# Kernel tuning notes

Hardware: AMD Instinct MI355X
Metric: run time of the kernel (lower is better)

Reference implementation:

```python
import jax, jax.numpy as jnp
import numpy as np

# Problem sizes (batched graph of G molecules)
N = 100_000   # total nodes
E = 400_000   # total directed edges
G = 2_500     # number of molecule graphs
K = 3         # len(idx_wo_smiles) -> zero rows inserted
NODE_F = 74   # graph_feats_shape[0]
EDGE_F = 12   # graph_feats_shape[1]
HID = 128     # hidden_feats = dim // 2
DIM = 256     # dim


def setup_inputs() -> dict:
    key = jax.random.key(0)
    ks = jax.random.split(key, 20)
    init = lambda k, shape, fan: (jax.random.normal(k, shape, jnp.float32) / np.sqrt(fan)).astype(jnp.float32)

    node_feats = jax.random.normal(ks[0], (N, NODE_F), jnp.float32)
    edge_feats = jax.random.normal(ks[1], (E, EDGE_F), jnp.float32)  # passed but unused by GCN
    src = jax.random.randint(ks[2], (E,), 0, N)
    dst = jax.random.randint(ks[3], (E,), 0, N)
    # sorted graph ids, every graph non-empty (~40 atoms each)
    graph_ids = (jnp.arange(N) * G) // N
    idx_wo_smiles = jnp.arange(K)

    return {
        'node_feats': node_feats,
        'edge_feats': edge_feats,
        'W1': init(ks[4], (NODE_F, HID), NODE_F), 'b1': jnp.zeros((HID,), jnp.float32),
        'Wr1': init(ks[5], (NODE_F, HID), NODE_F), 'br1': jnp.zeros((HID,), jnp.float32),
        'W2': init(ks[6], (HID, HID), HID), 'b2': jnp.zeros((HID,), jnp.float32),
        'Wr2': init(ks[7], (HID, HID), HID), 'br2': jnp.zeros((HID,), jnp.float32),
        'w_atom': init(ks[8], (HID, 1), HID), 'b_atom': jnp.zeros((1,), jnp.float32),
        'Wp1': init(ks[9], (2 * HID, HID), 2 * HID), 'bp1': jnp.zeros((HID,), jnp.float32),
        'Wp2': init(ks[10], (HID, DIM), HID), 'bp2': jnp.zeros((DIM,), jnp.float32),
        'src': src, 'dst': dst, 'graph_ids': graph_ids, 'idx_wo_smiles': idx_wo_smiles,
    }


def reference(node_feats, edge_feats, W1, b1, Wr1, br1, W2, b2, Wr2, br2,
              w_atom, b_atom, Wp1, bp1, Wp2, bp2, src, dst, graph_ids, idx_wo_smiles):
    n = node_feats.shape[0]
    ones_e = jnp.ones(src.shape[0], jnp.float32)
    out_deg = jax.ops.segment_sum(ones_e, src, num_segments=n)
    in_deg = jax.ops.segment_sum(ones_e, dst, num_segments=n)
    norm_s = jax.lax.rsqrt(jnp.maximum(out_deg, 1.0))  # [N]
    norm_d = jax.lax.rsqrt(jnp.maximum(in_deg, 1.0))   # [N]

    def gcn_layer(h, W, b, Wr, br):
        # GraphConv(norm='both'): D^-1/2 A D^-1/2 h W + b, with relu activation
        m = h[src] * norm_s[src][:, None]                       # [E, F] gather
        agg = jax.ops.segment_sum(m, dst, num_segments=n)       # [N, F] scatter-add
        gc = jax.nn.relu((agg * norm_d[:, None]) @ W + b)
        res = jax.nn.relu(h @ Wr + br)                          # residual connection
        return gc + res

    h = gcn_layer(node_feats, W1, b1, Wr1, br1)   # [N, HID]
    h = gcn_layer(h, W2, b2, Wr2, br2)            # [N, HID]

    # WeightedSumAndMax readout per molecule
    aw = jax.nn.sigmoid(h @ w_atom + b_atom)                          # [N, 1]
    hsum = jax.ops.segment_sum(h * aw, graph_ids, num_segments=G)     # [G, HID]
    hmax = jax.ops.segment_max(h, graph_ids, num_segments=G)          # [G, HID]
    gfeat = jnp.concatenate([hsum, hmax], axis=1)                     # [G, 2*HID]

    latent = jax.nn.relu(gfeat @ Wp1 + bp1) @ Wp2 + bp2               # [G, DIM]

    # Insert zero rows at idx_wo_smiles (sorted ascending -> final positions)
    total = G + idx_wo_smiles.shape[0]
    zero_mask = jnp.zeros((total,), bool).at[idx_wo_smiles].set(True)
    keep = jnp.nonzero(~zero_mask, size=G)[0]
    out = jnp.zeros((total, latent.shape[1]), latent.dtype).at[keep].set(latent)
    return out
```

## Files before the change

kernel.cpp:

```cpp
#include <hip/hip_runtime.h>
#include <hip/hip_bf16.h>

#define NODE_F 74
#define HID 128
#define DIM 256

typedef __hip_bfloat16 bf16;
typedef unsigned int u32;
typedef unsigned short u16;

typedef short s16x8 __attribute__((ext_vector_type(8)));
typedef __bf16 bf16x8 __attribute__((ext_vector_type(8)));
typedef float f32x4 __attribute__((ext_vector_type(4)));

__device__ __forceinline__ float rdl(float v, int l){
  return __int_as_float(__builtin_amdgcn_readlane(__float_as_int(v), l));
}
__device__ __forceinline__ float2 bfpair(u32 u){
  float2 r;
  r.x = __uint_as_float(u << 16);
  r.y = __uint_as_float(u & 0xffff0000u);
  return r;
}
__device__ __forceinline__ u16 bfbits(float a){
  return __bfloat16_as_ushort(__float2bfloat16(a));
}

__global__ void k_deg(const int* __restrict__ src, const int* __restrict__ dst,
                      float* __restrict__ outdeg_f, int* __restrict__ indeg, int E_){
  int e = blockIdx.x*256 + threadIdx.x;
  if (e < E_){
    atomicAdd(&outdeg_f[src[e]], 1.0f);
    atomicAdd(&indeg[dst[e]], 1);
  }
}

__global__ void k_norm(float* __restrict__ norm_s, const int* __restrict__ indeg,
                       float* __restrict__ norm_d, int n){
  int i = blockIdx.x*256 + threadIdx.x;
  if (i < n){
    norm_s[i] = rsqrtf(fmaxf(norm_s[i], 1.0f));
    norm_d[i] = rsqrtf(fmaxf((float)indeg[i], 1.0f));
  }
}

__global__ __launch_bounds__(256) void k_scan_a(const int* __restrict__ indeg,
                                                int* __restrict__ bsum, int n){
  __shared__ int red[256];
  const int base = blockIdx.x*1024 + threadIdx.x*4;
  int s = 0;
  #pragma unroll
  for (int i = 0; i < 4; ++i){
    const int idx = base + i;
    s += (idx < n) ? indeg[idx] : 0;
  }
  red[threadIdx.x] = s;
  __syncthreads();
  #pragma unroll
  for (int off = 128; off; off >>= 1){
    if (threadIdx.x < off) red[threadIdx.x] += red[threadIdx.x + off];
    __syncthreads();
  }
  if (threadIdx.x == 0) bsum[blockIdx.x] = red[0];
}

__global__ __launch_bounds__(1024) void k_scan_b(int* __restrict__ bsum, int nb){
  __shared__ int part[1024];
  __shared__ int carry;
  if (threadIdx.x == 0) carry = 0;
  __syncthreads();
  for (int c0 = 0; c0 < nb; c0 += 1024){
    const int tid = threadIdx.x, idx = c0 + tid;
    part[tid] = (idx < nb) ? bsum[idx] : 0;
    __syncthreads();
    for (int off = 1; off < 1024; off <<= 1){
      const int t = (tid >= off) ? part[tid-off] : 0;
      __syncthreads();
      part[tid] += t;
      __syncthreads();
    }
    if (idx < nb) bsum[idx] = carry + ((tid == 0) ? 0 : part[tid-1]);
    __syncthreads();
    if (tid == 0) carry += part[1023];
    __syncthreads();
  }
}

__global__ __launch_bounds__(256) void k_scan_c(int* __restrict__ indeg,
                                                const int* __restrict__ bsum,
                                                int* __restrict__ row_ptr, int n){
  __shared__ int part[256];
  const int base = blockIdx.x*1024 + threadIdx.x*4;
  int v[4]; int s = 0;
  #pragma unroll
  for (int i = 0; i < 4; ++i){
    const int idx = base + i;
    v[i] = (idx < n) ? indeg[idx] : 0;
    s += v[i];
  }
  part[threadIdx.x] = s;
  __syncthreads();
  for (int off = 1; off < 256; off <<= 1){
    const int t = (threadIdx.x >= off) ? part[threadIdx.x-off] : 0;
    __syncthreads();
    part[threadIdx.x] += t;
    __syncthreads();
  }
  int run = bsum[blockIdx.x] + ((threadIdx.x == 0) ? 0 : part[threadIdx.x-1]);
  #pragma unroll
  for (int i = 0; i < 4; ++i){
    const int idx = base + i;
    if (idx < n){
      row_ptr[idx] = run;
      run += v[i];
      indeg[idx] = 0;
    }
    if (idx == n-1) row_ptr[n] = run;
  }
}

__global__ void k_fill(const int* __restrict__ src, const int* __restrict__ dst,
                       const int* __restrict__ row_ptr, int* __restrict__ cursor,
                       int* __restrict__ col, int E_){
  int e = blockIdx.x*256 + threadIdx.x;
  if (e < E_){
    int d = dst[e];
    int pos = row_ptr[d] + atomicAdd(&cursor[d], 1);
    col[pos] = src[e];
  }
}

__global__ void k_prep(const float* __restrict__ W, u16* __restrict__ dst,
                       int S, int Ktrue){
  int idx = blockIdx.x*256 + threadIdx.x;
  const int tot = 8*S*512;
  if (idx >= tot) return;
  const int e   = idx & 7;
  const int l   = (idx >> 3) & 63;
  const int rem = idx >> 9;
  const int s   = rem % S;
  const int t   = rem / S;
  const int k   = s*32 + (l >> 4)*8 + e;
  const int c   = t*16 + (l & 15);
  const float v = (k < Ktrue) ? W[(size_t)k*HID + c] : 0.f;
  dst[idx] = bfbits(v);
}

__global__ __launch_bounds__(256) void k_fgemm1(
    const float* __restrict__ x0, const int* __restrict__ row_ptr,
    const int* __restrict__ col, const float* __restrict__ norm_s,
    const float* __restrict__ norm_d,
    const u16* __restrict__ Bp, const float* __restrict__ bg_,
    const float* __restrict__ br_, u16* __restrict__ h1, int n){
  const int lane = threadIdx.x & 63;
  const int wid  = threadIdx.x >> 6;
  const int jg = lane & 15, kg = lane >> 4;
  const int r0 = blockIdx.x*64 + wid*16;
  const int row = r0 + jg;
  const bool rok = row < n;
  const int kb = kg*8;

  float agg[3][8];
  #pragma unroll
  for (int s = 0; s < 3; ++s)
    #pragma unroll
    for (int e = 0; e < 8; ++e) agg[s][e] = 0.f;

  auto accum = [&](const float* px, float ns){
    #pragma unroll
    for (int s = 0; s < 2; ++s){
      #pragma unroll
      for (int e = 0; e < 8; e += 2){
        const float2 v = *(const float2*)&px[s*32 + kb + e];
        agg[s][e]   = fmaf(v.x, ns, agg[s][e]);
        agg[s][e+1] = fmaf(v.y, ns, agg[s][e+1]);
      }
    }
    if (kg == 0){
      #pragma unroll
      for (int e = 0; e < 8; e += 2){
        const float2 v = *(const float2*)&px[64 + e];
        agg[2][e]   = fmaf(v.x, ns, agg[2][e]);
        agg[2][e+1] = fmaf(v.y, ns, agg[2][e+1]);
      }
    } else if (kg == 1){
      const float2 v = *(const float2*)&px[72];
      agg[2][0] = fmaf(v.x, ns, agg[2][0]);
      agg[2][1] = fmaf(v.y, ns, agg[2][1]);
    }
  };

  int p0 = 0, p1 = 0;
  if (rok){ p0 = row_ptr[row]; p1 = row_ptr[row+1]; }
  int p = p0;
  #pragma unroll 1
  for (; p + 1 < p1; p += 2){
    const int sa = col[p], sb = col[p+1];
    const float na = norm_s[sa], nb = norm_s[sb];
    const float* xa = x0 + (size_t)sa*NODE_F;
    const float* xb = x0 + (size_t)sb*NODE_F;
    accum(xa, na);
    accum(xb, nb);
  }
  if (p < p1){
    const int sa = col[p];
    accum(x0 + (size_t)sa*NODE_F, norm_s[sa]);
  }

  const float nd = rok ? norm_d[row] : 0.f;
  bf16x8 ag[3], ar[3];
  #pragma unroll
  for (int s = 0; s < 3; ++s)
    #pragma unroll
    for (int e = 0; e < 8; ++e) ag[s][e] = (__bf16)(agg[s][e]*nd);

  {
    const int rA = rok ? row : (n-1);
    const float* px = x0 + (size_t)rA*NODE_F;
    #pragma unroll
    for (int s = 0; s < 2; ++s)
      #pragma unroll
      for (int e = 0; e < 8; e += 2){
        const float2 w = *(const float2*)&px[s*32 + kb + e];
        ar[s][e]   = (__bf16)w.x;
        ar[s][e+1] = (__bf16)w.y;
      }
    #pragma unroll
    for (int e = 0; e < 8; ++e) ar[2][e] = (__bf16)0.f;
    if (kg == 0){
      #pragma unroll
      for (int e = 0; e < 8; e += 2){
        const float2 w = *(const float2*)&px[64 + e];
        ar[2][e]   = (__bf16)w.x;
        ar[2][e+1] = (__bf16)w.y;
      }
    } else if (kg == 1){
      const float2 w = *(const float2*)&px[72];
      ar[2][0] = (__bf16)w.x;
      ar[2][1] = (__bf16)w.y;
    }
  }

  f32x4 accg[8], accr[8];
  #pragma unroll
  for (int t = 0; t < 8; ++t){
    accg[t] = f32x4{0.f,0.f,0.f,0.f};
    accr[t] = f32x4{0.f,0.f,0.f,0.f};
  }
  constexpr int FR1 = 8*3*512;
  #pragma unroll
  for (int s = 0; s < 3; ++s){
    #pragma unroll
    for (int t = 0; t < 8; ++t){
      const bf16x8 bg = __builtin_bit_cast(bf16x8,
          *(const s16x8*)&Bp[((t*3 + s)*64 + lane)*8]);
      const bf16x8 br = __builtin_bit_cast(bf16x8,
          *(const s16x8*)&Bp[FR1 + ((t*3 + s)*64 + lane)*8]);
      accg[t] = __builtin_amdgcn_mfma_f32_16x16x32_bf16(ag[s], bg, accg[t], 0,0,0);
      accr[t] = __builtin_amdgcn_mfma_f32_16x16x32_bf16(ar[s], br, accr[t], 0,0,0);
    }
  }

  const int rowb = r0 + 4*kg;
  #pragma unroll
  for (int t = 0; t < 8; ++t){
    const int colc = t*16 + jg;
    const float bgv = bg_[colc], brv = br_[colc];
    #pragma unroll
    for (int r = 0; r < 4; ++r){
      const int row2 = rowb + r;
      if (row2 < n){
        const float o = fmaxf(accg[t][r] + bgv, 0.f) + fmaxf(accr[t][r] + brv, 0.f);
        h1[(size_t)row2*HID + colc] = bfbits(o);
      }
    }
  }
}

__global__ __launch_bounds__(256) void k_fgemm2(
    const u16* __restrict__ h1, const int* __restrict__ row_ptr,
    const int* __restrict__ col, const float* __restrict__ norm_s,
    const float* __restrict__ norm_d,
    const u16* __restrict__ Bp, const float* __restrict__ bg_,
    const float* __restrict__ br_,
    const float* __restrict__ w_atom, const float* __restrict__ b_atom,
    const int* __restrict__ gid,
    float* __restrict__ hsum, u32* __restrict__ hmax, int n){
  const int lane = threadIdx.x & 63;
  const int wid  = threadIdx.x >> 6;
  const int jg = lane & 15, kg = lane >> 4;
  const int r0 = blockIdx.x*64 + wid*16;
  const int row = r0 + jg;
  const bool rok = row < n;
  const int kb = kg*8;

  float agg[4][8];
  #pragma unroll
  for (int s = 0; s < 4; ++s)
    #pragma unroll
    for (int e = 0; e < 8; ++e) agg[s][e] = 0.f;

  auto accum = [&](uint4 v, int s, float ns){
    const float2 f0 = bfpair(v.x), f1 = bfpair(v.y);
    const float2 f2 = bfpair(v.z), f3 = bfpair(v.w);
    agg[s][0] = fmaf(f0.x, ns, agg[s][0]);
    agg[s][1] = fmaf(f0.y, ns, agg[s][1]);
    agg[s][2] = fmaf(f1.x, ns, agg[s][2]);
    agg[s][3] = fmaf(f1.y, ns, agg[s][3]);
    agg[s][4] = fmaf(f2.x, ns, agg[s][4]);
    agg[s][5] = fmaf(f2.y, ns, agg[s][5]);
    agg[s][6] = fmaf(f3.x, ns, agg[s][6]);
    agg[s][7] = fmaf(f3.y, ns, agg[s][7]);
  };

  int p0 = 0, p1 = 0;
  if (rok){ p0 = row_ptr[row]; p1 = row_ptr[row+1]; }
  int p = p0;
  #pragma unroll 1
  for (; p + 1 < p1; p += 2){
    const int sa = col[p], sb = col[p+1];
    const float na = norm_s[sa], nb = norm_s[sb];
    const u16* pa = h1 + (size_t)sa*HID + kb;
    const u16* pb = h1 + (size_t)sb*HID + kb;
    const uint4 va0 = *(const uint4*)(pa);
    const uint4 va1 = *(const uint4*)(pa + 32);
    const uint4 va2 = *(const uint4*)(pa + 64);
    const uint4 va3 = *(const uint4*)(pa + 96);
    const uint4 vb0 = *(const uint4*)(pb);
    const uint4 vb1 = *(const uint4*)(pb + 32);
    const uint4 vb2 = *(const uint4*)(pb + 64);
    const uint4 vb3 = *(const uint4*)(pb + 96);
    accum(va0, 0, na); accum(va1, 1, na); accum(va2, 2, na); accum(va3, 3, na);
    accum(vb0, 0, nb); accum(vb1, 1, nb); accum(vb2, 2, nb); accum(vb3, 3, nb);
  }
  if (p < p1){
    const int sa = col[p];
    const float na = norm_s[sa];
    const u16* pa = h1 + (size_t)sa*HID + kb;
    accum(*(const uint4*)(pa),      0, na);
    accum(*(const uint4*)(pa + 32), 1, na);
    accum(*(const uint4*)(pa + 64), 2, na);
    accum(*(const uint4*)(pa + 96), 3, na);
  }

  const float nd = rok ? norm_d[row] : 0.f;
  bf16x8 ag[4];
  #pragma unroll
  for (int s = 0; s < 4; ++s)
    #pragma unroll
    for (int e = 0; e < 8; ++e) ag[s][e] = (__bf16)(agg[s][e]*nd);

  const int rA = rok ? row : (n-1);
  const u16* phr = h1 + (size_t)rA*HID + kb;

  f32x4 accg[8], accr[8];
  #pragma unroll
  for (int t = 0; t < 8; ++t){
    accg[t] = f32x4{0.f,0.f,0.f,0.f};
    accr[t] = f32x4{0.f,0.f,0.f,0.f};
  }
  constexpr int FR2 = 8*4*512;
  #pragma unroll
  for (int s = 0; s < 4; ++s){
    const bf16x8 arf = __builtin_bit_cast(bf16x8, *(const s16x8*)(phr + s*32));
    #pragma unroll
    for (int t = 0; t < 8; ++t){
      const bf16x8 bg = __builtin_bit_cast(bf16x8,
          *(const s16x8*)&Bp[((t*4 + s)*64 + lane)*8]);
      const bf16x8 br = __builtin_bit_cast(bf16x8,
          *(const s16x8*)&Bp[FR2 + ((t*4 + s)*64 + lane)*8]);
      accg[t] = __builtin_amdgcn_mfma_f32_16x16x32_bf16(ag[s], bg, accg[t], 0,0,0);
      accr[t] = __builtin_amdgcn_mfma_f32_16x16x32_bf16(arf, br, accr[t], 0,0,0);
    }
  }

  float o[8][4];
  #pragma unroll
  for (int t = 0; t < 8; ++t){
    const int colc = t*16 + jg;
    const float bgv = bg_[colc], brv = br_[colc];
    #pragma unroll
    for (int r = 0; r < 4; ++r)
      o[t][r] = fmaxf(accg[t][r] + bgv, 0.f) + fmaxf(accr[t][r] + brv, 0.f);
  }
  if (r0 < n){
    float wa[8];
    #pragma unroll
    for (int t = 0; t < 8; ++t) wa[t] = w_atom[t*16 + jg];
    const float ba = b_atom[0];
    const int rowb = r0 + 4*kg;
    float awv[4]; int gidr[4];
    #pragma unroll
    for (int r = 0; r < 4; ++r){
      const int row2 = rowb + r;
      float dot = 0.f;
      #pragma unroll
      for (int t = 0; t < 8; ++t) dot = fmaf(o[t][r], wa[t], dot);
      dot += __shfl_xor(dot, 1);
      dot += __shfl_xor(dot, 2);
      dot += __shfl_xor(dot, 4);
      dot += __shfl_xor(dot, 8);
      awv[r]  = 1.0f/(1.0f + __expf(-(dot + ba)));
      gidr[r] = (row2 < n) ? gid[row2] : -1;
    }
    const int rhi    = (r0 + 15 < n) ? (r0 + 15) : (n - 1);
    const int gfirst = gid[r0];
    const int glast  = gid[rhi];
    for (int g = gfirst; g <= glast; ++g){
      #pragma unroll
      for (int t = 0; t < 8; ++t){
        float sv = 0.f, mv = 0.f;
        #pragma unroll
        for (int r = 0; r < 4; ++r){
          const bool in = (gidr[r] == g);
          sv += in ? o[t][r]*awv[r] : 0.f;
          mv  = in ? fmaxf(mv, o[t][r]) : mv;
        }
        sv += __shfl_xor(sv, 16);
        sv += __shfl_xor(sv, 32);
        mv  = fmaxf(mv, __shfl_xor(mv, 16));
        mv  = fmaxf(mv, __shfl_xor(mv, 32));
        if (lane < 16){
          atomicAdd(&hsum[(size_t)g*HID + t*16 + jg], sv);
          atomicMax(&hmax[(size_t)g*HID + t*16 + jg], __float_as_uint(mv));
        }
      }
    }
  }
}

__global__ __launch_bounds__(256) void k_mlp1(
    const float* __restrict__ hsum, const float* __restrict__ hmaxf,
    const float* __restrict__ Wp1, const float* __restrict__ bp1,
    float* __restrict__ hid, int G_){
  const int lane = threadIdx.x & 63;
  const int row = blockIdx.x*4 + (threadIdx.x >> 6);
  if (row >= G_) return;
  const int c = lane*2;
  float ra0 = hsum[(size_t)row*HID + lane];
  float ra1 = hsum[(size_t)row*HID + 64 + lane];
  float ra2 = hmaxf[(size_t)row*HID + lane];
  float ra3 = hmaxf[(size_t)row*HID + 64 + lane];
  float a0 = 0.f, a1 = 0.f;
  #pragma unroll 4
  for (int k = 0; k < 64; ++k){
    const float v0 = rdl(ra0,k), v1 = rdl(ra1,k), v2 = rdl(ra2,k), v3 = rdl(ra3,k);
    const float2 w0 = *(const float2*)&Wp1[(size_t)(k      )*HID + c];
    const float2 w1 = *(const float2*)&Wp1[(size_t)(k +  64)*HID + c];
    const float2 w2 = *(const float2*)&Wp1[(size_t)(k + 128)*HID + c];
    const float2 w3 = *(const float2*)&Wp1[(size_t)(k + 192)*HID + c];
    a0 = fmaf(v0,w0.x, fmaf(v1,w1.x, fmaf(v2,w2.x, fmaf(v3,w3.x, a0))));
    a1 = fmaf(v0,w0.y, fmaf(v1,w1.y, fmaf(v2,w2.y, fmaf(v3,w3.y, a1))));
  }
  hid[(size_t)row*HID + c]   = fmaxf(a0 + bp1[c],   0.f);
  hid[(size_t)row*HID + c+1] = fmaxf(a1 + bp1[c+1], 0.f);
}

__global__ __launch_bounds__(256) void k_mlp2(
    const float* __restrict__ hid, const float* __restrict__ Wp2,
    const float* __restrict__ bp2, const int* __restrict__ idxw, int K_,
    float* __restrict__ out, int G_){
  const int lane = threadIdx.x & 63;
  const int row = blockIdx.x*4 + (threadIdx.x >> 6);
  if (row >= G_) return;
  const int c = lane*4;
  float ra0 = hid[(size_t)row*HID + lane];
  float ra1 = hid[(size_t)row*HID + 64 + lane];
  float acc0=0.f, acc1=0.f, acc2=0.f, acc3=0.f;
  #pragma unroll 4
  for (int k = 0; k < 64; ++k){
    const float a = rdl(ra0, k);
    const float4 w = *(const float4*)&Wp2[(size_t)k*DIM + c];
    acc0 = fmaf(a,w.x,acc0); acc1 = fmaf(a,w.y,acc1);
    acc2 = fmaf(a,w.z,acc2); acc3 = fmaf(a,w.w,acc3);
  }
  #pragma unroll 4
  for (int k = 64; k < 128; ++k){
    const float a = rdl(ra1, k-64);
    const float4 w = *(const float4*)&Wp2[(size_t)k*DIM + c];
    acc0 = fmaf(a,w.x,acc0); acc1 = fmaf(a,w.y,acc1);
    acc2 = fmaf(a,w.z,acc2); acc3 = fmaf(a,w.w,acc3);
  }
  int orow = row;
  for (int j = 0; j < K_; ++j){ if (idxw[j] <= orow) orow++; }
  float* po = out + (size_t)orow*DIM + c;
  po[0] = acc0 + bp2[c];
  po[1] = acc1 + bp2[c+1];
  po[2] = acc2 + bp2[c+2];
  po[3] = acc3 + bp2[c+3];
}

extern "C" void kernel_launch(void* const* d_in, const int* in_sizes, int n_in,
                              void* d_out, int out_size, void* d_ws, size_t ws_size,
                              hipStream_t stream){
  (void)n_in; (void)ws_size;
  const float* x0     = (const float*)d_in[0];
  const float* W1     = (const float*)d_in[2];
  const float* b1     = (const float*)d_in[3];
  const float* Wr1    = (const float*)d_in[4];
  const float* br1    = (const float*)d_in[5];
  const float* W2     = (const float*)d_in[6];
  const float* b2     = (const float*)d_in[7];
  const float* Wr2    = (const float*)d_in[8];
  const float* br2    = (const float*)d_in[9];
  const float* w_atom = (const float*)d_in[10];
  const float* b_atom = (const float*)d_in[11];
  const float* Wp1    = (const float*)d_in[12];
  const float* bp1    = (const float*)d_in[13];
  const float* Wp2    = (const float*)d_in[14];
  const float* bp2    = (const float*)d_in[15];
  const int* src  = (const int*)d_in[16];
  const int* dst  = (const int*)d_in[17];
  const int* gid  = (const int*)d_in[18];
  const int* idxw = (const int*)d_in[19];

  const int N_ = in_sizes[0] / NODE_F;
  const int E_ = in_sizes[16];
  const int K_ = in_sizes[19];
  const int G_ = out_size / DIM - K_;

  u16*   h1     = (u16*)d_ws;
  float* norm_s = (float*)(h1 + (size_t)N_*HID);
  float* norm_d = norm_s + N_;
  float* hsum   = norm_d + N_;
  float* hmaxv  = hsum + (size_t)G_*HID;
  float* hid    = hmaxv + (size_t)G_*HID;
  int*   indeg  = (int*)(hid + (size_t)G_*HID);
  int*   row_ptr= indeg + N_;
  int*   col    = row_ptr + ((N_ + 4) & ~3);
  int*   bsum   = col + ((E_ + 4) & ~3);
  u16*   Bp1    = (u16*)d_out;
  u16*   Bp2    = Bp1 + 2*8*3*512;

  hipMemsetAsync(norm_s, 0, (size_t)2*N_*sizeof(float), stream);
  hipMemsetAsync(hsum, 0, (size_t)2*G_*HID*sizeof(float), stream);
  hipMemsetAsync(indeg, 0, (size_t)N_*sizeof(int), stream);

  const int nscan = (N_ + 1023)/1024;
  k_deg   <<<(E_+255)/256, 256, 0, stream>>>(src, dst, norm_s, indeg, E_);
  k_norm  <<<(N_+255)/256, 256, 0, stream>>>(norm_s, indeg, norm_d, N_);
  k_scan_a<<<nscan, 256, 0, stream>>>(indeg, bsum, N_);
  k_scan_b<<<1, 1024, 0, stream>>>(bsum, nscan);
  k_scan_c<<<nscan, 256, 0, stream>>>(indeg, bsum, row_ptr, N_);
  k_fill  <<<(E_+255)/256, 256, 0, stream>>>(src, dst, row_ptr, indeg, col, E_);

  k_prep<<<(8*3*512+255)/256, 256, 0, stream>>>(W1,  Bp1,            3, NODE_F);
  k_prep<<<(8*3*512+255)/256, 256, 0, stream>>>(Wr1, Bp1 + 8*3*512,  3, NODE_F);
  k_prep<<<(8*4*512+255)/256, 256, 0, stream>>>(W2,  Bp2,            4, HID);
  k_prep<<<(8*4*512+255)/256, 256, 0, stream>>>(Wr2, Bp2 + 8*4*512,  4, HID);

  const int nb = (N_ + 63) / 64;
  k_fgemm1<<<nb, 256, 0, stream>>>(x0, row_ptr, col, norm_s, norm_d,
                                   Bp1, b1, br1, h1, N_);
  k_fgemm2<<<nb, 256, 0, stream>>>(h1, row_ptr, col, norm_s, norm_d,
                                   Bp2, b2, br2, w_atom, b_atom, gid,
                                   hsum, (u32*)hmaxv, N_);

  hipMemsetAsync(d_out, 0, (size_t)out_size*sizeof(float), stream);

  k_mlp1<<<(G_+3)/4, 256, 0, stream>>>(hsum, hmaxv, Wp1, bp1, hid, G_);
  k_mlp2<<<(G_+3)/4, 256, 0, stream>>>(hid, Wp2, bp2, idxw, K_, (float*)d_out, G_);
}
```

Before: 367.7 us.

## Fuse small kernels and memsets, and unroll the neighbor gather loops by four

The rsqrt degree normalisation moves into the first scan pass, and the four weight-prep launches become one kernel. The two readout MLP kernels merge into one, which drops the intermediate hidden buffer. The three workspace memsets become a single memset over a reordered contiguous layout, and the full output memset is replaced by zeroing only the inserted rows inside the MLP kernel. The CSR gather loops in both GCN layers now process four neighbors per iteration to expose more memory-level parallelism, at the cost of some extra register pressure.

After: 366.7 us. About the same (-0.3%).

```diff
diff --git a/kernel.cpp b/kernel.cpp
--- a/kernel.cpp
+++ b/kernel.cpp
@@ -35,16 +35,9 @@
   }
 }
 
-__global__ void k_norm(float* __restrict__ norm_s, const int* __restrict__ indeg,
-                       float* __restrict__ norm_d, int n){
-  int i = blockIdx.x*256 + threadIdx.x;
-  if (i < n){
-    norm_s[i] = rsqrtf(fmaxf(norm_s[i], 1.0f));
-    norm_d[i] = rsqrtf(fmaxf((float)indeg[i], 1.0f));
-  }
-}
-
 __global__ __launch_bounds__(256) void k_scan_a(const int* __restrict__ indeg,
+                                                float* __restrict__ norm_s,
+                                                float* __restrict__ norm_d,
                                                 int* __restrict__ bsum, int n){
   __shared__ int red[256];
   const int base = blockIdx.x*1024 + threadIdx.x*4;
@@ -52,7 +45,12 @@
   #pragma unroll
   for (int i = 0; i < 4; ++i){
     const int idx = base + i;
-    s += (idx < n) ? indeg[idx] : 0;
+    if (idx < n){
+      const int d = indeg[idx];
+      s += d;
+      norm_d[idx] = rsqrtf(fmaxf((float)d, 1.0f));
+      norm_s[idx] = rsqrtf(fmaxf(norm_s[idx], 1.0f));
+    }
   }
   red[threadIdx.x] = s;
   __syncthreads();
@@ -130,20 +128,26 @@
   }
 }
 
-__global__ void k_prep(const float* __restrict__ W, u16* __restrict__ dst,
-                       int S, int Ktrue){
+__global__ __launch_bounds__(256) void k_prep_all(
+    const float* __restrict__ W1, const float* __restrict__ Wr1,
+    const float* __restrict__ W2, const float* __restrict__ Wr2,
+    u16* __restrict__ Bp1, u16* __restrict__ Bp2){
   int idx = blockIdx.x*256 + threadIdx.x;
-  const int tot = 8*S*512;
-  if (idx >= tot) return;
-  const int e   = idx & 7;
-  const int l   = (idx >> 3) & 63;
-  const int rem = idx >> 9;
+  const float* W; u16* dst; int S, Ktrue, loc;
+  if      (idx < 12288){ W = W1;  dst = Bp1;          S = 3; Ktrue = NODE_F; loc = idx; }
+  else if (idx < 24576){ W = Wr1; dst = Bp1 + 12288;  S = 3; Ktrue = NODE_F; loc = idx - 12288; }
+  else if (idx < 40960){ W = W2;  dst = Bp2;          S = 4; Ktrue = HID;    loc = idx - 24576; }
+  else if (idx < 57344){ W = Wr2; dst = Bp2 + 16384;  S = 4; Ktrue = HID;    loc = idx - 40960; }
+  else return;
+  const int e   = loc & 7;
+  const int l   = (loc >> 3) & 63;
+  const int rem = loc >> 9;
   const int s   = rem % S;
   const int t   = rem / S;
   const int k   = s*32 + (l >> 4)*8 + e;
   const int c   = t*16 + (l & 15);
   const float v = (k < Ktrue) ? W[(size_t)k*HID + c] : 0.f;
-  dst[idx] = bfbits(v);
+  dst[loc] = bfbits(v);
 }
 
 __global__ __launch_bounds__(256) void k_fgemm1(
@@ -194,17 +198,24 @@
   if (rok){ p0 = row_ptr[row]; p1 = row_ptr[row+1]; }
   int p = p0;
   #pragma unroll 1
+  for (; p + 3 < p1; p += 4){
+    const int s0 = col[p], s1 = col[p+1], s2 = col[p+2], s3 = col[p+3];
+    const float n0 = norm_s[s0], n1 = norm_s[s1], n2 = norm_s[s2], n3 = norm_s[s3];
+    accum(x0 + (size_t)s0*NODE_F, n0);
+    accum(x0 + (size_t)s1*NODE_F, n1);
+    accum(x0 + (size_t)s2*NODE_F, n2);
+    accum(x0 + (size_t)s3*NODE_F, n3);
+  }
+  #pragma unroll 1
   for (; p + 1 < p1; p += 2){
-    const int sa = col[p], sb = col[p+1];
-    const float na = norm_s[sa], nb = norm_s[sb];
-    const float* xa = x0 + (size_t)sa*NODE_F;
-    const float* xb = x0 + (size_t)sb*NODE_F;
-    accum(xa, na);
-    accum(xb, nb);
+    const int s0 = col[p], s1 = col[p+1];
+    const float n0 = norm_s[s0], n1 = norm_s[s1];
+    accum(x0 + (size_t)s0*NODE_F, n0);
+    accum(x0 + (size_t)s1*NODE_F, n1);
   }
   if (p < p1){
-    const int sa = col[p];
-    accum(x0 + (size_t)sa*NODE_F, norm_s[sa]);
+    const int s0 = col[p];
+    accum(x0 + (size_t)s0*NODE_F, norm_s[s0]);
   }
 
   const float nd = rok ? norm_d[row] : 0.f;
@@ -312,35 +323,36 @@
     agg[s][6] = fmaf(f3.x, ns, agg[s][6]);
     agg[s][7] = fmaf(f3.y, ns, agg[s][7]);
   };
+  auto gatherN = [&](const u16* ph, float ns){
+    const uint4 v0 = *(const uint4*)(ph);
+    const uint4 v1 = *(const uint4*)(ph + 32);
+    const uint4 v2 = *(const uint4*)(ph + 64);
+    const uint4 v3 = *(const uint4*)(ph + 96);
+    accum(v0, 0, ns); accum(v1, 1, ns); accum(v2, 2, ns); accum(v3, 3, ns);
+  };
 
   int p0 = 0, p1 = 0;
   if (rok){ p0 = row_ptr[row]; p1 = row_ptr[row+1]; }
   int p = p0;
   #pragma unroll 1
+  for (; p + 3 < p1; p += 4){
+    const int s0 = col[p], s1 = col[p+1], s2 = col[p+2], s3 = col[p+3];
+    const float n0 = norm_s[s0], n1 = norm_s[s1], n2 = norm_s[s2], n3 = norm_s[s3];
+    gatherN(h1 + (size_t)s0*HID + kb, n0);
+    gatherN(h1 + (size_t)s1*HID + kb, n1);
+    gatherN(h1 + (size_t)s2*HID + kb, n2);
+    gatherN(h1 + (size_t)s3*HID + kb, n3);
+  }
+  #pragma unroll 1
   for (; p + 1 < p1; p += 2){
-    const int sa = col[p], sb = col[p+1];
-    const float na = norm_s[sa], nb = norm_s[sb];
-    const u16* pa = h1 + (size_t)sa*HID + kb;
-    const u16* pb = h1 + (size_t)sb*HID + kb;
-    const uint4 va0 = *(const uint4*)(pa);
-    const uint4 va1 = *(const uint4*)(pa + 32);
-    const uint4 va2 = *(const uint4*)(pa + 64);
-    const uint4 va3 = *(const uint4*)(pa + 96);
-    const uint4 vb0 = *(const uint4*)(pb);
-    const uint4 vb1 = *(const uint4*)(pb + 32);
-    const uint4 vb2 = *(const uint4*)(pb + 64);
-    const uint4 vb3 = *(const uint4*)(pb + 96);
-    accum(va0, 0, na); accum(va1, 1, na); accum(va2, 2, na); accum(va3, 3, na);
-    accum(vb0, 0, nb); accum(vb1, 1, nb); accum(vb2, 2, nb); accum(vb3, 3, nb);
+    const int s0 = col[p], s1 = col[p+1];
+    const float n0 = norm_s[s0], n1 = norm_s[s1];
+    gatherN(h1 + (size_t)s0*HID + kb, n0);
+    gatherN(h1 + (size_t)s1*HID + kb, n1);
   }
   if (p < p1){
-    const int sa = col[p];
-    const float na = norm_s[sa];
-    const u16* pa = h1 + (size_t)sa*HID + kb;
-    accum(*(const uint4*)(pa),      0, na);
-    accum(*(const uint4*)(pa + 32), 1, na);
-    accum(*(const uint4*)(pa + 64), 2, na);
-    accum(*(const uint4*)(pa + 96), 3, na);
+    const int s0 = col[p];
+    gatherN(h1 + (size_t)s0*HID + kb, norm_s[s0]);
   }
 
   const float nd = rok ? norm_d[row] : 0.f;
@@ -429,16 +441,25 @@
   }
 }
 
-__global__ __launch_bounds__(256) void k_mlp1(
+__global__ __launch_bounds__(256) void k_mlp(
     const float* __restrict__ hsum, const float* __restrict__ hmaxf,
     const float* __restrict__ Wp1, const float* __restrict__ bp1,
-    float* __restrict__ hid, int G_){
+    const float* __restrict__ Wp2, const float* __restrict__ bp2,
+    const int* __restrict__ idxw, int K_,
+    float* __restrict__ out, int G_){
   const int lane = threadIdx.x & 63;
   const int row = blockIdx.x*4 + (threadIdx.x >> 6);
+  if (blockIdx.x == 0){
+    for (int j = 0; j < K_; ++j){
+      const int zr = idxw[j];
+      for (int i = threadIdx.x; i < DIM; i += 256)
+        out[(size_t)zr*DIM + i] = 0.f;
+    }
+  }
   if (row >= G_) return;
   const int c = lane*2;
-  float ra0 = hsum[(size_t)row*HID + lane];
-  float ra1 = hsum[(size_t)row*HID + 64 + lane];
+  float ra0 = hsum [(size_t)row*HID + lane];
+  float ra1 = hsum [(size_t)row*HID + 64 + lane];
   float ra2 = hmaxf[(size_t)row*HID + lane];
   float ra3 = hmaxf[(size_t)row*HID + 64 + lane];
   float a0 = 0.f, a1 = 0.f;
@@ -452,42 +473,28 @@
     a0 = fmaf(v0,w0.x, fmaf(v1,w1.x, fmaf(v2,w2.x, fmaf(v3,w3.x, a0))));
     a1 = fmaf(v0,w0.y, fmaf(v1,w1.y, fmaf(v2,w2.y, fmaf(v3,w3.y, a1))));
   }
-  hid[(size_t)row*HID + c]   = fmaxf(a0 + bp1[c],   0.f);
-  hid[(size_t)row*HID + c+1] = fmaxf(a1 + bp1[c+1], 0.f);
-}
-
-__global__ __launch_bounds__(256) void k_mlp2(
-    const float* __restrict__ hid, const float* __restrict__ Wp2,
-    const float* __restrict__ bp2, const int* __restrict__ idxw, int K_,
-    float* __restrict__ out, int G_){
-  const int lane = threadIdx.x & 63;
-  const int row = blockIdx.x*4 + (threadIdx.x >> 6);
-  if (row >= G_) return;
-  const int c = lane*4;
-  float ra0 = hid[(size_t)row*HID + lane];
-  float ra1 = hid[(size_t)row*HID + 64 + lane];
+  const float h0  = fmaxf(a0 + bp1[c],   0.f);
+  const float h1v = fmaxf(a1 + bp1[c+1], 0.f);
+  const int c4 = lane*4;
   float acc0=0.f, acc1=0.f, acc2=0.f, acc3=0.f;
   #pragma unroll 4
-  for (int k = 0; k < 64; ++k){
-    const float a = rdl(ra0, k);
-    const float4 w = *(const float4*)&Wp2[(size_t)k*DIM + c];
-    acc0 = fmaf(a,w.x,acc0); acc1 = fmaf(a,w.y,acc1);
-    acc2 = fmaf(a,w.z,acc2); acc3 = fmaf(a,w.w,acc3);
-  }
-  #pragma unroll 4
-  for (int k = 64; k < 128; ++k){
-    const float a = rdl(ra1, k-64);
-    const float4 w = *(const float4*)&Wp2[(size_t)k*DIM + c];
-    acc0 = fmaf(a,w.x,acc0); acc1 = fmaf(a,w.y,acc1);
-    acc2 = fmaf(a,w.z,acc2); acc3 = fmaf(a,w.w,acc3);
+  for (int j = 0; j < 64; ++j){
+    const float he = rdl(h0, j);
+    const float ho = rdl(h1v, j);
+    const float4 we = *(const float4*)&Wp2[(size_t)(2*j  )*DIM + c4];
+    const float4 wo = *(const float4*)&Wp2[(size_t)(2*j+1)*DIM + c4];
+    acc0 = fmaf(he,we.x, fmaf(ho,wo.x, acc0));
+    acc1 = fmaf(he,we.y, fmaf(ho,wo.y, acc1));
+    acc2 = fmaf(he,we.z, fmaf(ho,wo.z, acc2));
+    acc3 = fmaf(he,we.w, fmaf(ho,wo.w, acc3));
   }
   int orow = row;
   for (int j = 0; j < K_; ++j){ if (idxw[j] <= orow) orow++; }
-  float* po = out + (size_t)orow*DIM + c;
-  po[0] = acc0 + bp2[c];
-  po[1] = acc1 + bp2[c+1];
-  po[2] = acc2 + bp2[c+2];
-  po[3] = acc3 + bp2[c+3];
+  float* po = out + (size_t)orow*DIM + c4;
+  po[0] = acc0 + bp2[c4];
+  po[1] = acc1 + bp2[c4+1];
+  po[2] = acc2 + bp2[c4+2];
+  po[3] = acc3 + bp2[c4+3];
 }
 
 extern "C" void kernel_launch(void* const* d_in, const int* in_sizes, int n_in,
@@ -520,34 +527,26 @@
   const int G_ = out_size / DIM - K_;
 
   u16*   h1     = (u16*)d_ws;
-  float* norm_s = (float*)(h1 + (size_t)N_*HID);
-  float* norm_d = norm_s + N_;
-  float* hsum   = norm_d + N_;
+  float* norm_d = (float*)(h1 + (size_t)N_*HID);
+  float* norm_s = norm_d + N_;
+  float* hsum   = norm_s + N_;
   float* hmaxv  = hsum + (size_t)G_*HID;
-  float* hid    = hmaxv + (size_t)G_*HID;
-  int*   indeg  = (int*)(hid + (size_t)G_*HID);
+  int*   indeg  = (int*)(hmaxv + (size_t)G_*HID);
   int*   row_ptr= indeg + N_;
   int*   col    = row_ptr + ((N_ + 4) & ~3);
   int*   bsum   = col + ((E_ + 4) & ~3);
   u16*   Bp1    = (u16*)d_out;
-  u16*   Bp2    = Bp1 + 2*8*3*512;
-
-  hipMemsetAsync(norm_s, 0, (size_t)2*N_*sizeof(float), stream);
-  hipMemsetAsync(hsum, 0, (size_t)2*G_*HID*sizeof(float), stream);
-  hipMemsetAsync(indeg, 0, (size_t)N_*sizeof(int), stream);
+  u16*   Bp2    = Bp1 + 2*12288;
+
+  hipMemsetAsync(norm_s, 0, ((size_t)2*N_ + (size_t)2*G_*HID)*sizeof(float), stream);
 
   const int nscan = (N_ + 1023)/1024;
-  k_deg   <<<(E_+255)/256, 256, 0, stream>>>(src, dst, norm_s, indeg, E_);
-  k_norm  <<<(N_+255)/256, 256, 0, stream>>>(norm_s, indeg, norm_d, N_);
-  k_scan_a<<<nscan, 256, 0, stream>>>(indeg, bsum, N_);
-  k_scan_b<<<1, 1024, 0, stream>>>(bsum, nscan);
-  k_scan_c<<<nscan, 256, 0, stream>>>(indeg, bsum, row_ptr, N_);
-  k_fill  <<<(E_+255)/256, 256, 0, stream>>>(src, dst, row_ptr, indeg, col, E_);
-
-  k_prep<<<(8*3*512+255)/256, 256, 0, stream>>>(W1,  Bp1,            3, NODE_F);
-  k_prep<<<(8*3*512+255)/256, 256, 0, stream>>>(Wr1, Bp1 + 8*3*512,  3, NODE_F);
-  k_prep<<<(8*4*512+255)/256, 256, 0, stream>>>(W2,  Bp2,            4, HID);
-  k_prep<<<(8*4*512+255)/256, 256, 0, stream>>>(Wr2, Bp2 + 8*4*512,  4, HID);
+  k_deg     <<<(E_+255)/256, 256, 0, stream>>>(src, dst, norm_s, indeg, E_);
+  k_scan_a  <<<nscan, 256, 0, stream>>>(indeg, norm_s, norm_d, bsum, N_);
+  k_scan_b  <<<1, 1024, 0, stream>>>(bsum, nscan);
+  k_scan_c  <<<nscan, 256, 0, stream>>>(indeg, bsum, row_ptr, N_);
+  k_fill    <<<(E_+255)/256, 256, 0, stream>>>(src, dst, row_ptr, indeg, col, E_);
+  k_prep_all<<<(57344+255)/256, 256, 0, stream>>>(W1, Wr1, W2, Wr2, Bp1, Bp2);
 
   const int nb = (N_ + 63) / 64;
   k_fgemm1<<<nb, 256, 0, stream>>>(x0, row_ptr, col, norm_s, norm_d,
@@ -556,8 +555,6 @@
                                    Bp2, b2, br2, w_atom, b_atom, gid,
                                    hsum, (u32*)hmaxv, N_);
 
-  hipMemsetAsync(d_out, 0, (size_t)out_size*sizeof(float), stream);
-
-  k_mlp1<<<(G_+3)/4, 256, 0, stream>>>(hsum, hmaxv, Wp1, bp1, hid, G_);
-  k_mlp2<<<(G_+3)/4, 256, 0, stream>>>(hid, Wp2, bp2, idxw, K_, (float*)d_out, G_);
-}
+  k_mlp<<<(G_+3)/4, 256, 0, stream>>>(hsum, hmaxv, Wp1, bp1, Wp2, bp2,
+                                      idxw, K_, (float*)d_out, G_);
+}
```
